# Kernel optimization log

Hardware: AMD Instinct MI355X
Metric: run time of the kernel (lower is better)

Reference implementation:

```python
import jax, jax.numpy as jnp
import numpy as np
import math

NUM_BUCKETS = 32
MAX_DISTANCE = 128
N_HEADS = 16
D_KV = 64


def _relative_position_bucket(relative_position, num_buckets=NUM_BUCKETS, max_distance=MAX_DISTANCE):
    # bidirectional (encoder) variant: is_decoder=False
    nb = num_buckets // 2
    rel_buckets = (relative_position > 0).astype(jnp.int32) * nb
    rp = jnp.abs(relative_position)
    max_exact = nb // 2
    is_small = rp < max_exact
    rp_large = max_exact + (
        jnp.log(rp.astype(jnp.float32) / max_exact)
        / math.log(max_distance / max_exact)
        * (nb - max_exact)
    ).astype(jnp.int32)
    rp_large = jnp.minimum(rp_large, nb - 1)
    return rel_buckets + jnp.where(is_small, rp, rp_large)


def compute_position_bias(rel_bias_table, q_len, k_len):
    ctx = jnp.arange(q_len, dtype=jnp.int32)[:, None]
    mem = jnp.arange(k_len, dtype=jnp.int32)[None, :]
    buckets = _relative_position_bucket(mem - ctx)  # [q_len, k_len]
    values = rel_bias_table[buckets]                # [q_len, k_len, H]
    return jnp.transpose(values, (2, 0, 1))[None]   # [1, H, q_len, k_len]


def setup_inputs() -> dict:
    key = jax.random.key(0)
    ks = jax.random.split(key, 6)
    B, S, D = 2, 2048, 1024
    s = 0.02
    return {
        "hidden_states": jax.random.normal(ks[0], (B, S, D), dtype=jnp.float32),
        "Wq": jax.random.normal(ks[1], (D, N_HEADS * D_KV), dtype=jnp.float32) * s,
        "Wk": jax.random.normal(ks[2], (D, N_HEADS * D_KV), dtype=jnp.float32) * s,
        "Wv": jax.random.normal(ks[3], (D, N_HEADS * D_KV), dtype=jnp.float32) * s,
        "Wo": jax.random.normal(ks[4], (N_HEADS * D_KV, D), dtype=jnp.float32) * s,
        "rel_bias_table": jax.random.normal(ks[5], (NUM_BUCKETS, N_HEADS), dtype=jnp.float32),
    }


def reference(hidden_states, Wq, Wk, Wv, Wo, rel_bias_table):
    B, S, D = hidden_states.shape
    H, dh = N_HEADS, D_KV
    q = (hidden_states @ Wq).reshape(B, S, H, dh)
    k = (hidden_states @ Wk).reshape(B, S, H, dh)
    v = (hidden_states @ Wv).reshape(B, S, H, dh)

    position_bias = compute_position_bias(rel_bias_table, S, S)  # [1,H,S,S]

    scale = 1.0 / math.sqrt(dh)  # applied inside optimized_attention (SDPA convention)
    scores = jnp.einsum('bqhd,bkhd->bhqk', q, k) * scale + position_bias
    probs = jax.nn.softmax(scores, axis=-1)
    ctx = jnp.einsum('bhqk,bkhd->bqhd', probs, v).reshape(B, S, H * dh)
    attn_output = ctx @ Wo
    return attn_output
```

## Files before the change

### kernel.cpp

```cpp
#include <hip/hip_runtime.h>

typedef __attribute__((ext_vector_type(8))) short s16x8;
typedef __attribute__((ext_vector_type(4))) short s16x4;
typedef __attribute__((ext_vector_type(4))) float f32x4;
typedef __attribute__((ext_vector_type(4))) unsigned int u32x4;
typedef __attribute__((ext_vector_type(2))) unsigned int u32x2;
typedef unsigned short u16;
typedef unsigned int u32;

#define LOG2E 1.4426950408889634f

__device__ __forceinline__ u16 f2bf(float x) {
  u32 u = __float_as_uint(x);
  u += 0x7FFFu + ((u >> 16) & 1u);
  return (u16)(u >> 16);
}

__device__ __forceinline__ float bf2f(u16 x) {
  return __uint_as_float((u32)x << 16);
}

__device__ __forceinline__ u32 pack_bf_trunc(float lo, float hi) {
  return (__float_as_uint(lo) >> 16) | (__float_as_uint(hi) & 0xFFFF0000u);
}

__device__ __forceinline__ void gl_lds16(const void* g, void* l) {
  __builtin_amdgcn_global_load_lds((const __attribute__((address_space(1))) void*)g,
                                   (__attribute__((address_space(3))) void*)l, 16, 0, 0);
}

#define MFMA16(a, b, c) __builtin_amdgcn_mfma_f32_16x16x32_bf16((a), (b), (c), 0, 0, 0)


__global__ __launch_bounds__(256) void prep(const float* __restrict__ hs,
                                            const float* __restrict__ Wq,
                                            const float* __restrict__ Wk,
                                            const float* __restrict__ Wv,
                                            const float* __restrict__ Wo,
                                            const float* __restrict__ tbl,
                                            u16* __restrict__ hsb,
                                            u16* __restrict__ wt,
                                            u16* __restrict__ wot,
                                            float* __restrict__ biasT) {
  const int blk = blockIdx.x;
  const int tid = threadIdx.x;
  if (blk < 2048) {
    const int i = blk * 256 + tid;
    const float4* s4 = (const float4*)hs;
    float4 a = s4[i * 2];
    float4 b = s4[i * 2 + 1];
    s16x8 o;
    o[0] = (short)f2bf(a.x); o[1] = (short)f2bf(a.y);
    o[2] = (short)f2bf(a.z); o[3] = (short)f2bf(a.w);
    o[4] = (short)f2bf(b.x); o[5] = (short)f2bf(b.y);
    o[6] = (short)f2bf(b.z); o[7] = (short)f2bf(b.w);
    *(s16x8*)&hsb[i * 8] = o;
  } else if (blk < 4096) {
    int r = blk - 2048;
    const int sel = r >> 9;
    r &= 511;
    const float* W = sel == 0 ? Wq : (sel == 1 ? Wk : (sel == 2 ? Wv : Wo));
    u16* dst = sel == 3 ? wot : wt + sel * 1048576;
    const int n = (r & 15) * 64 + (tid & 63);
    const int kb = (r >> 4) * 32 + (tid >> 6) * 8;
    s16x8 o;
#pragma unroll
    for (int j = 0; j < 8; ++j) o[j] = (short)f2bf(W[(kb + j) * 1024 + n]);
    *(s16x8*)&dst[n * 1024 + kb] = o;
  } else {
    const int i = (blk - 4096) * 256 + tid;
    const int h = i >> 12, dp = i & 4095;
    const int delta = dp - 2047;
    const int rp = delta < 0 ? -delta : delta;
    int bucket = delta > 0 ? 16 : 0;
    if (rp < 8)
      bucket += rp;
    else
      bucket += 8 + (rp >= 12) + (rp >= 16) + (rp >= 23) + (rp >= 32) +
                (rp >= 46) + (rp >= 64) + (rp >= 91);
    biasT[i] = tbl[bucket * 16 + h] * LOG2E;
  }
}


__device__ __forceinline__ void gemm_core(const u16* __restrict__ A,
                                          const u16* __restrict__ Bt,
                                          int m0, int n0,
                                          u16* shbuf, f32x4 acc[4][4]) {
  const int tid = threadIdx.x;
  const int w = tid >> 6, l = tid & 63, g = l >> 4, m15 = l & 15;
  const int wr = (w >> 1) * 64, wc = (w & 1) * 64;
#pragma unroll
  for (int i = 0; i < 4; ++i)
#pragma unroll
    for (int j = 0; j < 4; ++j) acc[i][j] = (f32x4){0.f, 0.f, 0.f, 0.f};

#define GSTAGE(buf, k0)                                                    \
  {                                                                        \
    _Pragma("unroll") for (int c = 0; c < 2; ++c) {                        \
      const int idx = c * 256 + tid;                                       \
      const int row = idx >> 2, col4 = idx & 3;                            \
      const int scol = col4 ^ ((row >> 1) & 3);                            \
      gl_lds16(&A[(m0 + row) * 1024 + (k0) + scol * 8],                    \
               (char*)shbuf + (buf)*8192 + c * 4096 + w * 1024);           \
      gl_lds16(&Bt[(n0 + row) * 1024 + (k0) + scol * 8],                   \
               (char*)shbuf + 16384 + (buf)*8192 + c * 4096 + w * 1024);   \
    }                                                                      \
  }

  GSTAGE(0, 0);
  int cur = 0;
  for (int kt = 0; kt < 32; ++kt) {
    __syncthreads();
    if (kt < 31) GSTAGE(cur ^ 1, (kt + 1) * 32);
    const u16* Asb = shbuf + cur * 4096;
    const u16* Bsb = shbuf + 8192 + cur * 4096;
    s16x8 af[4], bfr[4];
#pragma unroll
    for (int mf = 0; mf < 4; ++mf) {
      const int row = wr + mf * 16 + m15;
      af[mf] = *(const s16x8*)&Asb[(row * 4 + (g ^ ((row >> 1) & 3))) * 8];
    }
#pragma unroll
    for (int nf = 0; nf < 4; ++nf) {
      const int row = wc + nf * 16 + m15;
      bfr[nf] = *(const s16x8*)&Bsb[(row * 4 + (g ^ ((row >> 1) & 3))) * 8];
    }
#pragma unroll
    for (int mf = 0; mf < 4; ++mf)
#pragma unroll
      for (int nf = 0; nf < 4; ++nf)
        acc[mf][nf] = MFMA16(af[mf], bfr[nf], acc[mf][nf]);
    cur ^= 1;
  }
#undef GSTAGE
}

__global__ __launch_bounds__(256) void gemm_qkv(const u16* __restrict__ X,
                                                const u16* __restrict__ Wt,
                                                u16* __restrict__ Q,
                                                u16* __restrict__ Kb,
                                                u16* __restrict__ VT) {
  __shared__ u16 shbuf[16384];
  f32x4 acc[4][4];
  const int flat = blockIdx.x;
  const int x = flat & 7, i = flat >> 3;
  const int m0 = ((x & 3) * 8 + (i & 7)) * 128;
  const int n0 = ((x >> 2) * 12 + (i >> 3)) * 128;
  gemm_core(X, Wt, m0, n0, shbuf, acc);

  const int tid = threadIdx.x;
  const int w = tid >> 6, l = tid & 63, g = l >> 4, m15 = l & 15;
  const int wr = (w >> 1) * 64, wc = (w & 1) * 64;
  const int nsel = n0 >> 10;
  const int ncol0 = (n0 & 1023) + wc;
  if (nsel == 2) {
    __syncthreads();
#pragma unroll
    for (int mf = 0; mf < 4; ++mf) {
      const int s_base = wr + mf * 16 + g * 4;
#pragma unroll
      for (int nf = 0; nf < 4; ++nf) {
        const int d_loc = wc + nf * 16 + m15;
        s16x4 pk;
#pragma unroll
        for (int r = 0; r < 4; ++r) pk[r] = (short)f2bf(acc[mf][nf][r]);
        *(s16x4*)&shbuf[d_loc * 128 + (s_base ^ ((d_loc & 7) << 3))] = pk;
      }
    }
    __syncthreads();
    const int b = m0 >> 11, sg0 = m0 & 2047;
#pragma unroll
    for (int it = 0; it < 8; ++it) {
      const int d_loc = it * 16 + w * 4 + g;
      const s16x8 v =
          *(const s16x8*)&shbuf[d_loc * 128 + ((m15 * 8) ^ ((d_loc & 7) << 3))];
      const int col = (n0 & 1023) + d_loc;
      *(s16x8*)&VT[((b * 16 + (col >> 6)) * 64 + (col & 63)) * 2048 + sg0 + m15 * 8] = v;
    }
  } else {
    u16* dst = nsel == 0 ? Q : Kb;
    const float scale = nsel == 0 ? 0.125f * LOG2E : 1.0f;
#pragma unroll
    for (int mf = 0; mf < 4; ++mf) {
      const int rbase = m0 + wr + mf * 16 + g * 4;
#pragma unroll
      for (int nf = 0; nf < 4; ++nf) {
        const int col = ncol0 + nf * 16 + m15;
#pragma unroll
        for (int r = 0; r < 4; ++r)
          dst[(rbase + r) * 1024 + col] = f2bf(acc[mf][nf][r] * scale);
      }
    }
  }
}

__global__ __launch_bounds__(256) void gemm_out(const u16* __restrict__ CTX,
                                                const u16* __restrict__ Wot,
                                                float* __restrict__ Out) {
  __shared__ u16 shbuf[16384];
  f32x4 acc[4][4];
  const int flat = blockIdx.x;
  const int x = flat & 7, i = flat >> 3;
  const int m0 = ((x & 3) * 8 + (i & 7)) * 128;
  const int n0 = ((x >> 2) * 4 + (i >> 3)) * 128;
  gemm_core(CTX, Wot, m0, n0, shbuf, acc);

  const int tid = threadIdx.x;
  const int w = tid >> 6, l = tid & 63, g = l >> 4, m15 = l & 15;
  const int wr = (w >> 1) * 64, wc = (w & 1) * 64;
#pragma unroll
  for (int mf = 0; mf < 4; ++mf) {
    const int rbase = m0 + wr + mf * 16 + g * 4;
#pragma unroll
    for (int nf = 0; nf < 4; ++nf) {
      const int col = n0 + wc + nf * 16 + m15;
#pragma unroll
      for (int r = 0; r < 4; ++r)
        Out[(rbase + r) * 1024 + col] = acc[mf][nf][r];
    }
  }
}


__global__ __launch_bounds__(256, 4) void attn_kernel(const u16* __restrict__ Qg,
                                                      const u16* __restrict__ Kg,
                                                      const u16* __restrict__ VTg,
                                                      const float* __restrict__ biasT,
                                                      const float* __restrict__ tbl,
                                                      u16* __restrict__ po0,
                                                      u16* __restrict__ po1,
                                                      float* __restrict__ pls) {
  __shared__ u16 KT[2][4096];
  __shared__ u16 VTs[2][4096];

  const int tid = threadIdx.x;
  const int w = tid >> 6, l = tid & 63, g = l >> 4, m15 = l & 15;
  const int flat = blockIdx.x;
  const int nf_ = (flat & 7) * 128 + (flat >> 3);
  const int bh = nf_ >> 5;
  const int rem = nf_ & 31;
  const int half = rem >> 4, qblk = rem & 15;
  const int b = bh >> 4, h = bh & 15;
  const int qw = qblk * 128 + w * 32;
  const int kvbase = half * 1024;

  u16* poh = half ? po1 : po0;
  float* plsh = pls + half * 65536;

  const float fpos = tbl[31 * 16 + h] * LOG2E;
  const float fneg = tbl[15 * 16 + h] * LOG2E;

  s16x8 aq[2][2];
#pragma unroll
  for (int qs = 0; qs < 2; ++qs) {
    const u16* qp = &Qg[(b * 2048 + qw + qs * 16 + m15) * 1024 + h * 64 + g * 8];
    aq[qs][0] = *(const s16x8*)qp;
    aq[qs][1] = *(const s16x8*)(qp + 32);
  }

  s16x8 vone;
#pragma unroll
  for (int j = 0; j < 8; ++j) vone[j] = (short)0x3F80;

  f32x4 o[2][4];
  f32x4 ls4[2];
#pragma unroll
  for (int qs = 0; qs < 2; ++qs) {
    ls4[qs] = (f32x4){0.f, 0.f, 0.f, 0.f};
#pragma unroll
    for (int d = 0; d < 4; ++d) o[qs][d] = (f32x4){0.f, 0.f, 0.f, 0.f};
  }

  const u16* Kbase = &Kg[(b * 2048 + kvbase) * 1024 + h * 64];
  const u16* Vbase = &VTg[bh * 64 * 2048 + kvbase];

#define STAGE(buf, kv0)                                                          \
  {                                                                              \
    _Pragma("unroll") for (int c = 0; c < 2; ++c) {                              \
      const int idx = c * 256 + tid;                                             \
      const int row = idx >> 3, col16 = idx & 7;                                 \
      const int scol = col16 ^ (row & 7);                                        \
      gl_lds16(&Kbase[(kv0 + row) * 1024 + scol * 8],                            \
               (char*)KT + (buf)*8192 + c * 4096 + w * 1024);                    \
      gl_lds16(&Vbase[row * 2048 + (kv0) + scol * 8],                            \
               (char*)VTs + (buf)*8192 + c * 4096 + w * 1024);                   \
    }                                                                            \
  }

  STAGE(0, 0);
  int cur = 0;
  for (int t = 0; t < 16; ++t) {
    const int kv0 = t * 64;
    __syncthreads();
    if (t < 15) STAGE(cur ^ 1, kv0 + 64);

    const u16* KTc = &KT[cur][0];
    const u16* VTc = &VTs[cur][0];

    f32x4 s[2][4];
    const int diff = kvbase + kv0 - qw;
    if (diff <= -160 || diff >= 128) {
      const float bc = diff > 0 ? fpos : fneg;
#pragma unroll
      for (int qs = 0; qs < 2; ++qs)
#pragma unroll
        for (int c = 0; c < 4; ++c) s[qs][c] = (f32x4){bc, bc, bc, bc};
    } else {
#pragma unroll
      for (int qs = 0; qs < 2; ++qs) {
        const float* bp =
            &biasT[h * 4096 + kvbase + kv0 + g * 4 - qw - qs * 16 - m15 + 2047];
#pragma unroll
        for (int c = 0; c < 4; ++c)
#pragma unroll
          for (int r = 0; r < 4; ++r) s[qs][c][r] = bp[c * 16 + r];
      }
    }

    __builtin_amdgcn_s_setprio(1);
#pragma unroll
    for (int ks = 0; ks < 2; ++ks) {
#pragma unroll
      for (int c = 0; c < 4; ++c) {
        const int row = c * 16 + m15;
        const s16x8 bk = *(const s16x8*)&KTc[(row * 8 + ((ks * 4 + g) ^ (row & 7))) * 8];
        s[0][c] = MFMA16(bk, aq[0][ks], s[0][c]);
        s[1][c] = MFMA16(bk, aq[1][ks], s[1][c]);
      }
    }
    __builtin_amdgcn_s_setprio(0);

    s16x8 pa[2][2];
#pragma unroll
    for (int qs = 0; qs < 2; ++qs) {
      u32 w01[4], w23[4];
#pragma unroll
      for (int c = 0; c < 4; ++c) {
        w01[c] = pack_bf_trunc(__builtin_amdgcn_exp2f(s[qs][c][0]),
                               __builtin_amdgcn_exp2f(s[qs][c][1]));
        w23[c] = pack_bf_trunc(__builtin_amdgcn_exp2f(s[qs][c][2]),
                               __builtin_amdgcn_exp2f(s[qs][c][3]));
      }
#pragma unroll
      for (int ks = 0; ks < 2; ++ks) {
        u32x2 rA = __builtin_amdgcn_permlane32_swap(w01[2 * ks], w01[2 * ks + 1], false, false);
        u32x2 rB = __builtin_amdgcn_permlane16_swap(rA[0], rA[1], false, false);
        u32x2 rC = __builtin_amdgcn_permlane32_swap(w23[2 * ks], w23[2 * ks + 1], false, false);
        u32x2 rD = __builtin_amdgcn_permlane16_swap(rC[0], rC[1], false, false);
        const u32x4 pd = (u32x4){rB[0], rD[0], rB[1], rD[1]};
        pa[qs][ks] = __builtin_bit_cast(s16x8, pd);
      }
    }

    __builtin_amdgcn_s_setprio(1);
#pragma unroll
    for (int ks = 0; ks < 2; ++ks) {
#pragma unroll
      for (int d = 0; d < 4; ++d) {
        const int rowv = d * 16 + m15;
        const s16x8 bv = *(const s16x8*)&VTc[(rowv * 8 + ((ks * 4 + g) ^ (rowv & 7))) * 8];
        o[0][d] = MFMA16(pa[0][ks], bv, o[0][d]);
        o[1][d] = MFMA16(pa[1][ks], bv, o[1][d]);
      }
      ls4[0] = MFMA16(pa[0][ks], vone, ls4[0]);
      ls4[1] = MFMA16(pa[1][ks], vone, ls4[1]);
    }
    __builtin_amdgcn_s_setprio(0);
    cur ^= 1;
  }
#undef STAGE

#pragma unroll
  for (int qs = 0; qs < 2; ++qs) {
    const int orow = b * 2048 + qw + qs * 16 + g * 4;
    const int ocol = h * 64 + m15;
#pragma unroll
    for (int r = 0; r < 4; ++r) {
#pragma unroll
      for (int d = 0; d < 4; ++d)
        poh[(orow + r) * 1024 + ocol + d * 16] = f2bf(o[qs][d][r]);
      if (m15 == 0) plsh[(orow + r) * 16 + h] = ls4[qs][r];
    }
  }
}

__global__ __launch_bounds__(256) void merge(const u16* __restrict__ po0,
                                             const u16* __restrict__ po1,
                                             const float* __restrict__ pls,
                                             u16* __restrict__ ctx) {
  const int i = blockIdx.x * 256 + threadIdx.x;
  const int row = i >> 7;
  const int seg = i & 127;
  const int h = seg >> 3;
  const float den = 1.0f / (pls[row * 16 + h] + pls[65536 + row * 16 + h]);
  const s16x8 a = *(const s16x8*)&po0[row * 1024 + seg * 8];
  const s16x8 b = *(const s16x8*)&po1[row * 1024 + seg * 8];
  s16x8 o;
#pragma unroll
  for (int j = 0; j < 8; ++j)
    o[j] = (short)f2bf((bf2f((u16)a[j]) + bf2f((u16)b[j])) * den);
  *(s16x8*)&ctx[row * 1024 + seg * 8] = o;
}


extern "C" void kernel_launch(void* const* d_in, const int* in_sizes, int n_in,
                              void* d_out, int out_size, void* d_ws, size_t ws_size,
                              hipStream_t stream) {
  (void)in_sizes; (void)n_in; (void)out_size; (void)ws_size;
  const float* hs  = (const float*)d_in[0];
  const float* Wq  = (const float*)d_in[1];
  const float* Wk  = (const float*)d_in[2];
  const float* Wv  = (const float*)d_in[3];
  const float* Wo  = (const float*)d_in[4];
  const float* tbl = (const float*)d_in[5];

  char* ws = (char*)d_ws;
  u16* hsb   = (u16*)(ws);
  u16* wt    = (u16*)(ws + 8388608);
  u16* wot   = (u16*)(ws + 14680064);
  u16* q     = (u16*)(ws + 16777216);
  u16* k     = (u16*)(ws + 25165824);
  u16* po0   = (u16*)(ws + 33554432);
  u16* vt    = (u16*)(ws + 41943040);
  u16* ctx   = (u16*)(ws + 50331648);
  float* biasT = (float*)(ws + 58720256);
  u16* po1   = hsb;
  float* pls = (float*)wt;

  prep<<<4352, 256, 0, stream>>>(hs, Wq, Wk, Wv, Wo, tbl, hsb, wt, wot, biasT);
  gemm_qkv<<<768, 256, 0, stream>>>(hsb, wt, q, k, vt);
  attn_kernel<<<1024, 256, 0, stream>>>(q, k, vt, biasT, tbl, po0, po1, pls);
  merge<<<2048, 256, 0, stream>>>(po0, po1, pls, ctx);
  gemm_out<<<256, 256, 0, stream>>>(ctx, wot, (float*)d_out);
}
```

Before: 120.7 us.

## Split attention KV range into four partitions and merge four partial outputs

The attention kernel now splits each head's key/value range into four 512-wide partitions instead of two 1024-wide ones. This doubles the grid to 2048 blocks and halves each block's KV loop. The merge kernel sums four partial outputs and denominators, writes the result in place into the first partial buffer, and borrows the final output buffer as scratch for the fourth partial. The bf16 truncating pack also switches to a single byte-permute builtin. The trade-off is more partial-output traffic, a heavier merge and more per-block prologue (Q loads, first stage) in exchange for finer-grained scheduling of the attention work.

Measured after the change: 123.0 us. About the same (+1.9%).

```diff
diff --git a/kernel.cpp b/kernel.cpp
--- a/kernel.cpp
+++ b/kernel.cpp
@@ -21,7 +21,7 @@
 }
 
 __device__ __forceinline__ u32 pack_bf_trunc(float lo, float hi) {
-  return (__float_as_uint(lo) >> 16) | (__float_as_uint(hi) & 0xFFFF0000u);
+  return __builtin_amdgcn_perm(__float_as_uint(hi), __float_as_uint(lo), 0x07060302u);
 }
 
 __device__ __forceinline__ void gl_lds16(const void* g, void* l) {
@@ -230,6 +230,8 @@
                                                       const float* __restrict__ tbl,
                                                       u16* __restrict__ po0,
                                                       u16* __restrict__ po1,
+                                                      u16* __restrict__ po2,
+                                                      u16* __restrict__ po3,
                                                       float* __restrict__ pls) {
   __shared__ u16 KT[2][4096];
   __shared__ u16 VTs[2][4096];
@@ -237,16 +239,16 @@
   const int tid = threadIdx.x;
   const int w = tid >> 6, l = tid & 63, g = l >> 4, m15 = l & 15;
   const int flat = blockIdx.x;
-  const int nf_ = (flat & 7) * 128 + (flat >> 3);
-  const int bh = nf_ >> 5;
-  const int rem = nf_ & 31;
-  const int half = rem >> 4, qblk = rem & 15;
+  const int nf_ = (flat & 7) * 256 + (flat >> 3);
+  const int bh = nf_ >> 6;
+  const int rem = nf_ & 63;
+  const int quarter = rem >> 4, qblk = rem & 15;
   const int b = bh >> 4, h = bh & 15;
   const int qw = qblk * 128 + w * 32;
-  const int kvbase = half * 1024;
-
-  u16* poh = half ? po1 : po0;
-  float* plsh = pls + half * 65536;
+  const int kvbase = quarter * 512;
+
+  u16* poh = quarter == 0 ? po0 : (quarter == 1 ? po1 : (quarter == 2 ? po2 : po3));
+  float* plsh = pls + quarter * 65536;
 
   const float fpos = tbl[31 * 16 + h] * LOG2E;
   const float fneg = tbl[15 * 16 + h] * LOG2E;
@@ -290,10 +292,10 @@
 
   STAGE(0, 0);
   int cur = 0;
-  for (int t = 0; t < 16; ++t) {
+  for (int t = 0; t < 8; ++t) {
     const int kv0 = t * 64;
     __syncthreads();
-    if (t < 15) STAGE(cur ^ 1, kv0 + 64);
+    if (t < 7) STAGE(cur ^ 1, kv0 + 64);
 
     const u16* KTc = &KT[cur][0];
     const u16* VTc = &VTs[cur][0];
@@ -385,22 +387,27 @@
   }
 }
 
-__global__ __launch_bounds__(256) void merge(const u16* __restrict__ po0,
-                                             const u16* __restrict__ po1,
-                                             const float* __restrict__ pls,
-                                             u16* __restrict__ ctx) {
+__global__ __launch_bounds__(256) void merge(const u16* po0, const u16* po1,
+                                             const u16* po2, const u16* po3,
+                                             const float* pls, u16* outp) {
   const int i = blockIdx.x * 256 + threadIdx.x;
   const int row = i >> 7;
   const int seg = i & 127;
   const int h = seg >> 3;
-  const float den = 1.0f / (pls[row * 16 + h] + pls[65536 + row * 16 + h]);
-  const s16x8 a = *(const s16x8*)&po0[row * 1024 + seg * 8];
-  const s16x8 b = *(const s16x8*)&po1[row * 1024 + seg * 8];
+  const int li = row * 16 + h;
+  const float den =
+      1.0f / (pls[li] + pls[65536 + li] + pls[131072 + li] + pls[196608 + li]);
+  const int base = row * 1024 + seg * 8;
+  const s16x8 a = *(const s16x8*)&po0[base];
+  const s16x8 b = *(const s16x8*)&po1[base];
+  const s16x8 c = *(const s16x8*)&po2[base];
+  const s16x8 d = *(const s16x8*)&po3[base];
   s16x8 o;
 #pragma unroll
   for (int j = 0; j < 8; ++j)
-    o[j] = (short)f2bf((bf2f((u16)a[j]) + bf2f((u16)b[j])) * den);
-  *(s16x8*)&ctx[row * 1024 + seg * 8] = o;
+    o[j] = (short)f2bf((bf2f((u16)a[j]) + bf2f((u16)b[j]) +
+                        bf2f((u16)c[j]) + bf2f((u16)d[j])) * den);
+  *(s16x8*)&outp[base] = o;
 }
 
 
@@ -423,14 +430,15 @@
   u16* k     = (u16*)(ws + 25165824);
   u16* po0   = (u16*)(ws + 33554432);
   u16* vt    = (u16*)(ws + 41943040);
-  u16* ctx   = (u16*)(ws + 50331648);
+  u16* po2   = (u16*)(ws + 50331648);
   float* biasT = (float*)(ws + 58720256);
   u16* po1   = hsb;
+  u16* po3   = (u16*)d_out;
   float* pls = (float*)wt;
 
   prep<<<4352, 256, 0, stream>>>(hs, Wq, Wk, Wv, Wo, tbl, hsb, wt, wot, biasT);
   gemm_qkv<<<768, 256, 0, stream>>>(hsb, wt, q, k, vt);
-  attn_kernel<<<1024, 256, 0, stream>>>(q, k, vt, biasT, tbl, po0, po1, pls);
-  merge<<<2048, 256, 0, stream>>>(po0, po1, pls, ctx);
-  gemm_out<<<256, 256, 0, stream>>>(ctx, wot, (float*)d_out);
-}
+  attn_kernel<<<2048, 256, 0, stream>>>(q, k, vt, biasT, tbl, po0, po1, po2, po3, pls);
+  merge<<<2048, 256, 0, stream>>>(po0, po1, po2, po3, pls, po0);
+  gemm_out<<<256, 256, 0, stream>>>(po0, wot, (float*)d_out);
+}
```

## Shrink output GEMM tile to 128x64 and double grid size

Applied to the files above, without the earlier changes.

The output projection GEMM now uses a dedicated 128x64 tile loop with its own double-buffered LDS staging instead of the shared 128x128 core, and launches 512 blocks instead of 256. With 256 blocks the grid roughly matches the CU count and gives poor latency hiding, so more, smaller blocks are meant to fill the GPU better. The cost is lower arithmetic intensity per block, meaning more global reloads of the A tile. Separately, bf16 truncation packing now uses a single v_perm byte-permute instead of a shift, mask and or.

After: 117.3 us (median of 2 runs). -2.8%, faster.

```diff
diff --git a/kernel.cpp b/kernel.cpp
--- a/kernel.cpp
+++ b/kernel.cpp
@@ -21,7 +21,7 @@
 }
 
 __device__ __forceinline__ u32 pack_bf_trunc(float lo, float hi) {
-  return (__float_as_uint(lo) >> 16) | (__float_as_uint(hi) & 0xFFFF0000u);
+  return __builtin_amdgcn_perm(__float_as_uint(hi), __float_as_uint(lo), 0x07060302u);
 }
 
 __device__ __forceinline__ void gl_lds16(const void* g, void* l) {
@@ -195,25 +195,75 @@
   }
 }
 
+
 __global__ __launch_bounds__(256) void gemm_out(const u16* __restrict__ CTX,
                                                 const u16* __restrict__ Wot,
                                                 float* __restrict__ Out) {
-  __shared__ u16 shbuf[16384];
-  f32x4 acc[4][4];
+  __shared__ u16 shbuf[12288];
+  f32x4 acc[4][2];
   const int flat = blockIdx.x;
   const int x = flat & 7, i = flat >> 3;
   const int m0 = ((x & 3) * 8 + (i & 7)) * 128;
-  const int n0 = ((x >> 2) * 4 + (i >> 3)) * 128;
-  gemm_core(CTX, Wot, m0, n0, shbuf, acc);
+  const int n0 = ((x >> 2) * 8 + (i >> 3)) * 64;
 
   const int tid = threadIdx.x;
   const int w = tid >> 6, l = tid & 63, g = l >> 4, m15 = l & 15;
-  const int wr = (w >> 1) * 64, wc = (w & 1) * 64;
+  const int wr = (w >> 1) * 64, wc = (w & 1) * 32;
+#pragma unroll
+  for (int mf = 0; mf < 4; ++mf)
+#pragma unroll
+    for (int nf = 0; nf < 2; ++nf) acc[mf][nf] = (f32x4){0.f, 0.f, 0.f, 0.f};
+
+#define OSTAGE(buf, k0)                                                    \
+  {                                                                        \
+    _Pragma("unroll") for (int c = 0; c < 2; ++c) {                        \
+      const int idx = c * 256 + tid;                                       \
+      const int row = idx >> 2, col4 = idx & 3;                            \
+      const int scol = col4 ^ ((row >> 1) & 3);                            \
+      gl_lds16(&CTX[(m0 + row) * 1024 + (k0) + scol * 8],                  \
+               (char*)shbuf + (buf)*8192 + c * 4096 + w * 1024);           \
+    }                                                                      \
+    {                                                                      \
+      const int row = tid >> 2, col4 = tid & 3;                            \
+      const int scol = col4 ^ ((row >> 1) & 3);                            \
+      gl_lds16(&Wot[(n0 + row) * 1024 + (k0) + scol * 8],                  \
+               (char*)shbuf + 16384 + (buf)*4096 + (w >> 1) * 2048 +       \
+                   (tid & 127) * 16);                                      \
+    }                                                                      \
+  }
+
+  OSTAGE(0, 0);
+  int cur = 0;
+  for (int kt = 0; kt < 32; ++kt) {
+    __syncthreads();
+    if (kt < 31) OSTAGE(cur ^ 1, (kt + 1) * 32);
+    const u16* Asb = shbuf + cur * 4096;
+    const u16* Bsb = shbuf + 8192 + cur * 2048;
+    s16x8 af[4], bfr[2];
+#pragma unroll
+    for (int mf = 0; mf < 4; ++mf) {
+      const int row = wr + mf * 16 + m15;
+      af[mf] = *(const s16x8*)&Asb[(row * 4 + (g ^ ((row >> 1) & 3))) * 8];
+    }
+#pragma unroll
+    for (int nf = 0; nf < 2; ++nf) {
+      const int row = wc + nf * 16 + m15;
+      bfr[nf] = *(const s16x8*)&Bsb[(row * 4 + (g ^ ((row >> 1) & 3))) * 8];
+    }
+#pragma unroll
+    for (int mf = 0; mf < 4; ++mf)
+#pragma unroll
+      for (int nf = 0; nf < 2; ++nf)
+        acc[mf][nf] = MFMA16(af[mf], bfr[nf], acc[mf][nf]);
+    cur ^= 1;
+  }
+#undef OSTAGE
+
 #pragma unroll
   for (int mf = 0; mf < 4; ++mf) {
     const int rbase = m0 + wr + mf * 16 + g * 4;
 #pragma unroll
-    for (int nf = 0; nf < 4; ++nf) {
+    for (int nf = 0; nf < 2; ++nf) {
       const int col = n0 + wc + nf * 16 + m15;
 #pragma unroll
       for (int r = 0; r < 4; ++r)
@@ -432,5 +482,5 @@
   gemm_qkv<<<768, 256, 0, stream>>>(hsb, wt, q, k, vt);
   attn_kernel<<<1024, 256, 0, stream>>>(q, k, vt, biasT, tbl, po0, po1, pls);
   merge<<<2048, 256, 0, stream>>>(po0, po1, pls, ctx);
-  gemm_out<<<256, 256, 0, stream>>>(ctx, wot, (float*)d_out);
-}
+  gemm_out<<<512, 256, 0, stream>>>(ctx, wot, (float*)d_out);
+}
```
